# Kernel tuning notes

Measured on AMD Instinct MI355X. Metric: run time of the kernel, lower is better.

The kernel has to match this reference:

```python
import jax, jax.numpy as jnp
import numpy as np

NENV, SEQ, LATENT = 4096, 128, 64
EMB, HID = 256, 1024
SA = 2  # state_action_size


def setup_inputs() -> dict:
    key = jax.random.key(0)
    ks = jax.random.split(key, 8)
    def w(k, shape):
        return (jax.random.normal(k, shape, jnp.float32) / np.sqrt(shape[0])).astype(jnp.float32)
    return {
        "z": jax.random.normal(ks[0], (NENV, SEQ, LATENT), jnp.float32),
        "rnn_hxs": jnp.zeros((NENV, HID), jnp.float32),
        "w1": w(ks[1], (SA + LATENT, 32)), "b1": jnp.zeros((32,), jnp.float32),
        "w2": w(ks[2], (32, EMB)),          "b2": jnp.zeros((EMB,), jnp.float32),
        "wih": w(ks[3], (EMB, 3 * HID)),    "bih": jnp.zeros((3 * HID,), jnp.float32),
        "whh": w(ks[4], (HID, 3 * HID)),    "bhh": jnp.zeros((3 * HID,), jnp.float32),
        "w3": w(ks[5], (HID, HID // 2)),    "b3": jnp.zeros((HID // 2,), jnp.float32),
        "w4": w(ks[6], (HID // 2, SA)),     "b4": jnp.zeros((SA,), jnp.float32),
    }


def _gru_cell(x, h, wih, whh, bih, bhh):
    # PyTorch nn.GRU single-step semantics.
    gi = x @ wih + bih                    # [n, 3H]
    gh = h @ whh + bhh                    # [n, 3H]
    i_r, i_z, i_n = jnp.split(gi, 3, axis=-1)
    h_r, h_z, h_n = jnp.split(gh, 3, axis=-1)
    r = jax.nn.sigmoid(i_r + h_r)
    u = jax.nn.sigmoid(i_z + h_z)
    n = jnp.tanh(i_n + r * h_n)
    return (1.0 - u) * n + u * h


def reference(z, rnn_hxs, w1, b1, w2, b2, wih, bih, whh, bhh, w3, b3, w4, b4):
    zt = jnp.transpose(z, (1, 0, 2))                     # [S, N, latent]
    state0 = -2.0 * jnp.ones((z.shape[0], SA), z.dtype)  # initial fake action/state

    def step(carry, z_t):
        state, h = carry
        x = jnp.concatenate([state, z_t], axis=-1)       # [N, 2+latent]
        x = jax.nn.relu(x @ w1 + b1)
        x = jax.nn.relu(x @ w2 + b2)                     # mlp_in -> [N, EMB]
        h = _gru_cell(x, h, wih, whh, bih, bhh)          # [N, HID]
        o = jax.nn.relu(h @ w3 + b3)
        o = jnp.tanh(o @ w4 + b4)                        # output_linear -> [N, 2]
        return (o, h), o

    (_, h_new), outs = jax.lax.scan(step, (state0, rnn_hxs), zt)
    # original returns outputs.permute(1,0,2) -> [nenv, seq, 2], plus new hidden
    return jnp.transpose(outs, (1, 0, 2)), h_new
```

## Files before the change

kernel.cpp:

```cpp
#include <hip/hip_runtime.h>
#include <cstdint>
#include <cstddef>

#define NENV 4096
#define SEQ  128
#define LATENT 64
#define EMB  256
#define HID  1024
#define SA   2

typedef _Float16 half8 __attribute__((ext_vector_type(8)));
typedef float f32x4 __attribute__((ext_vector_type(4)));

__device__ __forceinline__ float sigmoid_f(float x){ return 1.0f/(1.0f + __expf(-x)); }

__device__ __forceinline__ void dma16(const void* g, void* l){
  __builtin_amdgcn_global_load_lds(
      (const __attribute__((address_space(1))) void*)g,
      (__attribute__((address_space(3))) void*)l, 16, 0, 0);
}

__device__ __forceinline__ f32x4 mfma16(half8 a, half8 b, f32x4 c){
  return __builtin_amdgcn_mfma_f32_16x16x32_f16(a, b, c, 0, 0, 0);
}

__global__ void transpose_cvt_kernel(const float* __restrict__ in, _Float16* __restrict__ out,
                                     int K, int C){
  int n = K*C;
  for (int i = blockIdx.x*blockDim.x + threadIdx.x; i < n; i += gridDim.x*blockDim.x){
    int c = i / K;
    int k = i - c*K;
    out[i] = (_Float16)in[(size_t)k*C + c];
  }
}

__global__ void init_h_kernel(const float* __restrict__ rnn, _Float16* __restrict__ h16){
  int n = NENV*HID;
  for (int i = blockIdx.x*blockDim.x + threadIdx.x; i < n; i += gridDim.x*blockDim.x){
    h16[i] = (_Float16)rnn[i];
  }
}

__global__ __launch_bounds__(256, 4) void gru_kernel(
    const _Float16* __restrict__ x2h, const _Float16* __restrict__ hcur,
    const _Float16* __restrict__ wihT, const _Float16* __restrict__ whhT,
    const float* __restrict__ bih, const float* __restrict__ bhh,
    _Float16* __restrict__ hnxt, float* __restrict__ hout)
{
  __shared__ half8 sA[256];
  __shared__ half8 sB[3][256];
  const int tid = threadIdx.x;
  const int lane = tid & 63, wave = tid >> 6;
  const int m = lane & 15, q = lane >> 4, n0 = wave*16;
  const int row = tid >> 2, seg = tid & 3;

  const int id = blockIdx.x;
  const int colg = (id & 7)*2 + ((id >> 3) & 1);
  const int rowg = id >> 4;
  const int r0 = rowg*64, c0 = colg*64;

  f32x4 accR[4], accZ[4], accNi[4], accNh[4];
#pragma unroll
  for (int i = 0; i < 4; ++i){
    accR[i] = (f32x4){0.f,0.f,0.f,0.f};
    accZ[i] = (f32x4){0.f,0.f,0.f,0.f};
    accNi[i] = (f32x4){0.f,0.f,0.f,0.f};
    accNh[i] = (f32x4){0.f,0.f,0.f,0.f};
  }

  char* dA  = (char*)&sA[wave*64];
  char* dB0 = (char*)&sB[0][wave*64];
  char* dB1 = (char*)&sB[1][wave*64];
  char* dB2 = (char*)&sB[2][wave*64];

#pragma unroll
  for (int phase = 0; phase < 2; ++phase){
    const _Float16* A = phase ? hcur : x2h;
    const _Float16* W = phase ? whhT : wihT;
    const int K = phase ? HID : EMB;
    f32x4* accN = phase ? accNh : accNi;

    const _Float16* gA  = A + (size_t)(r0 + row)*K + seg*8;
    const _Float16* gB0 = W + (size_t)(0*HID + c0 + row)*K + seg*8;
    const _Float16* gB1 = W + (size_t)(1*HID + c0 + row)*K + seg*8;
    const _Float16* gB2 = W + (size_t)(2*HID + c0 + row)*K + seg*8;

    for (int k0 = 0; k0 < K; k0 += 32){
      dma16(gA, dA); dma16(gB0, dB0); dma16(gB1, dB1); dma16(gB2, dB2);
      gA += 32; gB0 += 32; gB1 += 32; gB2 += 32;
      __syncthreads();
      half8 b0 = sB[0][(n0+m)*4 + q];
      half8 b1 = sB[1][(n0+m)*4 + q];
      half8 b2 = sB[2][(n0+m)*4 + q];
#pragma unroll
      for (int mt = 0; mt < 4; ++mt){
        half8 a = sA[(mt*16 + m)*4 + q];
        accR[mt] = mfma16(a, b0, accR[mt]);
        accZ[mt] = mfma16(a, b1, accZ[mt]);
        accN[mt] = mfma16(a, b2, accN[mt]);
      }
      __syncthreads();
    }
  }

  const int gc = c0 + n0 + m;
  const float b_r  = bih[gc]         + bhh[gc];
  const float b_z  = bih[gc + HID]   + bhh[gc + HID];
  const float b_in = bih[gc + 2*HID];
  const float b_hn = bhh[gc + 2*HID];
#pragma unroll
  for (int mt = 0; mt < 4; ++mt){
#pragma unroll
    for (int r = 0; r < 4; ++r){
      int grow = r0 + mt*16 + q*4 + r;
      float rr = sigmoid_f(accR[mt][r] + b_r);
      float u  = sigmoid_f(accZ[mt][r] + b_z);
      float nn = tanhf(accNi[mt][r] + b_in + rr*(accNh[mt][r] + b_hn));
      size_t idx = (size_t)grow*HID + gc;
      float hold = (float)hcur[idx];
      float hnew = (1.0f - u)*nn + u*hold;
      hnxt[idx] = (_Float16)hnew;
      if (hout) hout[idx] = hnew;
    }
  }
}

__global__ __launch_bounds__(256, 4) void out1_kernel(
    const _Float16* __restrict__ h16, const _Float16* __restrict__ w3T,
    const float* __restrict__ b3, _Float16* __restrict__ o1)
{
  __shared__ half8 sA[256];
  __shared__ half8 sB[256];
  const int tid = threadIdx.x;
  const int lane = tid & 63, wave = tid >> 6;
  const int m = lane & 15, q = lane >> 4, n0 = wave*16;
  const int row = tid >> 2, seg = tid & 3;

  const int id = blockIdx.x;
  const int colg = id & 7;
  const int rowg = id >> 3;
  const int r0 = rowg*64, c0 = colg*64;

  f32x4 acc[4];
#pragma unroll
  for (int i = 0; i < 4; ++i) acc[i] = (f32x4){0.f,0.f,0.f,0.f};

  char* dA = (char*)&sA[wave*64];
  char* dB = (char*)&sB[wave*64];
  const _Float16* gA = h16 + (size_t)(r0 + row)*HID + seg*8;
  const _Float16* gB = w3T + (size_t)(c0 + row)*HID + seg*8;

  for (int k0 = 0; k0 < HID; k0 += 32){
    dma16(gA, dA); dma16(gB, dB);
    gA += 32; gB += 32;
    __syncthreads();
    half8 b = sB[(n0+m)*4 + q];
#pragma unroll
    for (int mt = 0; mt < 4; ++mt){
      half8 a = sA[(mt*16 + m)*4 + q];
      acc[mt] = mfma16(a, b, acc[mt]);
    }
    __syncthreads();
  }

  const int gc = c0 + n0 + m;
  const float bb = b3[gc];
#pragma unroll
  for (int mt = 0; mt < 4; ++mt){
#pragma unroll
    for (int r = 0; r < 4; ++r){
      int grow = r0 + mt*16 + q*4 + r;
      o1[(size_t)grow*(HID/2) + gc] = (_Float16)fmaxf(acc[mt][r] + bb, 0.f);
    }
  }
}

__global__ void tail_head_kernel(
    const _Float16* __restrict__ o1, const float* __restrict__ w4, const float* __restrict__ b4,
    const float* __restrict__ z,  const float* __restrict__ w1, const float* __restrict__ b1,
    const float* __restrict__ w2, const float* __restrict__ b2,
    _Float16* __restrict__ x2h, float* __restrict__ out, int t, int mode)
{
  __shared__ float sw2[32*256];
  __shared__ float sw1[66*32];
  __shared__ float sz[16][64];
  __shared__ float sx1[16][32];
  __shared__ float sst[16][2];
  const int tid = threadIdx.x;
  const int r0 = blockIdx.x*16;

  if (mode != 2){
    for (int i = tid; i < 66*32; i += 256) sw1[i] = w1[i];
    for (int i = tid; i < 32*256; i += 256) sw2[i] = w2[i];
    int zt = (mode == 0) ? 0 : (t + 1);
    for (int i = tid; i < 16*64; i += 256){
      int r = i >> 6, k = i & 63;
      sz[r][k] = z[(size_t)(r0 + r)*SEQ*LATENT + zt*LATENT + k];
    }
  }

  if (mode != 0){
    int r = tid >> 4, p = tid & 15;
    const _Float16* orow = o1 + (size_t)(r0 + r)*(HID/2);
    float a0 = 0.f, a1 = 0.f;
    for (int k = p*32; k < p*32 + 32; ++k){
      float v = (float)orow[k];
      a0 += v*w4[k*2];
      a1 += v*w4[k*2 + 1];
    }
#pragma unroll
    for (int off = 1; off < 16; off <<= 1){
      a0 += __shfl_xor(a0, off);
      a1 += __shfl_xor(a1, off);
    }
    if (p == 0){
      a0 = tanhf(a0 + b4[0]);
      a1 = tanhf(a1 + b4[1]);
      out[(size_t)(r0 + r)*SEQ*SA + t*SA + 0] = a0;
      out[(size_t)(r0 + r)*SEQ*SA + t*SA + 1] = a1;
      sst[r][0] = a0; sst[r][1] = a1;
    }
  } else {
    if (tid < 32) sst[tid >> 1][tid & 1] = -2.0f;
  }
  __syncthreads();

  if (mode != 2){
    for (int it = tid; it < 16*32; it += 256){
      int r = it >> 5, j = it & 31;
      float acc = b1[j];
      acc += sst[r][0]*sw1[0*32 + j] + sst[r][1]*sw1[1*32 + j];
#pragma unroll 8
      for (int k = 0; k < 64; ++k) acc += sz[r][k]*sw1[(k + 2)*32 + j];
      sx1[r][j] = fmaxf(acc, 0.f);
    }
    __syncthreads();
    int col = tid;
    for (int r = 0; r < 16; ++r){
      float acc = b2[col];
#pragma unroll
      for (int k = 0; k < 32; ++k) acc += sx1[r][k]*sw2[k*256 + col];
      x2h[(size_t)(r0 + r)*EMB + col] = (_Float16)fmaxf(acc, 0.f);
    }
  }
}

extern "C" void kernel_launch(void* const* d_in, const int* in_sizes, int n_in,
                              void* d_out, int out_size, void* d_ws, size_t ws_size,
                              hipStream_t stream) {
  const float* z   = (const float*)d_in[0];
  const float* rnn = (const float*)d_in[1];
  const float* w1  = (const float*)d_in[2];
  const float* b1  = (const float*)d_in[3];
  const float* w2  = (const float*)d_in[4];
  const float* b2  = (const float*)d_in[5];
  const float* wih = (const float*)d_in[6];
  const float* bih = (const float*)d_in[7];
  const float* whh = (const float*)d_in[8];
  const float* bhh = (const float*)d_in[9];
  const float* w3  = (const float*)d_in[10];
  const float* b3  = (const float*)d_in[11];
  const float* w4  = (const float*)d_in[12];
  const float* b4  = (const float*)d_in[13];
  float* out = (float*)d_out;

  char* ws = (char*)d_ws;
  _Float16* wihT = (_Float16*)ws;                 ws += (size_t)3*HID*EMB*2;
  _Float16* whhT = (_Float16*)ws;                 ws += (size_t)3*HID*HID*2;
  _Float16* w3T  = (_Float16*)ws;                 ws += (size_t)(HID/2)*HID*2;
  _Float16* h16a = (_Float16*)ws;                 ws += (size_t)NENV*HID*2;
  _Float16* h16b = (_Float16*)ws;                 ws += (size_t)NENV*HID*2;
  _Float16* x2h  = (_Float16*)ws;                 ws += (size_t)NENV*EMB*2;
  _Float16* o1   = (_Float16*)ws;                 ws += (size_t)NENV*(HID/2)*2;

  transpose_cvt_kernel<<<512, 256, 0, stream>>>(wih, wihT, EMB, 3*HID);
  transpose_cvt_kernel<<<1024, 256, 0, stream>>>(whh, whhT, HID, 3*HID);
  transpose_cvt_kernel<<<256, 256, 0, stream>>>(w3, w3T, HID, HID/2);
  init_h_kernel<<<1024, 256, 0, stream>>>(rnn, h16a);

  tail_head_kernel<<<NENV/16, 256, 0, stream>>>(o1, w4, b4, z, w1, b1, w2, b2, x2h, out, 0, 0);

  float* hfinal = out + (size_t)NENV*SEQ*SA;
  for (int t = 0; t < SEQ; ++t){
    _Float16* hc = (t & 1) ? h16b : h16a;
    _Float16* hn = (t & 1) ? h16a : h16b;
    gru_kernel<<<1024, 256, 0, stream>>>(x2h, hc, wihT, whhT, bih, bhh, hn,
                                         (t == SEQ - 1) ? hfinal : nullptr);
    out1_kernel<<<512, 256, 0, stream>>>(hn, w3T, b3, o1);
    tail_head_kernel<<<NENV/16, 256, 0, stream>>>(o1, w4, b4, z, w1, b1, w2, b2, x2h, out,
                                                  t, (t < SEQ - 1) ? 1 : 2);
  }
}
```

Baseline: 10.90 ms.

## Enlarge GRU and output GEMM tiles to 128 rows and 64-deep K steps

The GRU and first output-layer GEMM kernels now compute 128x64 output tiles instead of 64x64 and stage 64 elements of K per barrier pair instead of 32. Each weight fragment is reused across twice as many rows and there are half as many barriers per K sweep, cutting weight traffic and sync overhead. The cost is twice the accumulator registers (launch bounds lowered to 2 blocks), more LDS per block, and half as many blocks (512 and 256), which may leave some of the 256 CUs idle or lower occupancy.

```diff
diff --git a/kernel.cpp b/kernel.cpp
--- a/kernel.cpp
+++ b/kernel.cpp
@@ -41,67 +41,86 @@
   }
 }
 
-__global__ __launch_bounds__(256, 4) void gru_kernel(
+__device__ __forceinline__ void gru_phase(
+    const _Float16* __restrict__ A, const _Float16* __restrict__ W, int K,
+    int r0, int c0, int tid, int wave, int m, int q, int n0,
+    half8* sA, half8* sB, f32x4* accR, f32x4* accZ, f32x4* accN)
+{
+  const int row64 = tid >> 2, seg = tid & 3;
+  const _Float16* gA0 = A + (size_t)(r0 +  0 + row64)*K +  0 + seg*8;
+  const _Float16* gA1 = A + (size_t)(r0 + 64 + row64)*K +  0 + seg*8;
+  const _Float16* gA2 = A + (size_t)(r0 +  0 + row64)*K + 32 + seg*8;
+  const _Float16* gA3 = A + (size_t)(r0 + 64 + row64)*K + 32 + seg*8;
+  const _Float16* gB0 = W + (size_t)(0*HID + c0 + row64)*K +  0 + seg*8;
+  const _Float16* gB1 = W + (size_t)(0*HID + c0 + row64)*K + 32 + seg*8;
+  const _Float16* gB2 = W + (size_t)(1*HID + c0 + row64)*K +  0 + seg*8;
+  const _Float16* gB3 = W + (size_t)(1*HID + c0 + row64)*K + 32 + seg*8;
+  const _Float16* gB4 = W + (size_t)(2*HID + c0 + row64)*K +  0 + seg*8;
+  const _Float16* gB5 = W + (size_t)(2*HID + c0 + row64)*K + 32 + seg*8;
+
+  char* dA0 = (char*)&sA[0*256 + wave*64];
+  char* dA1 = (char*)&sA[1*256 + wave*64];
+  char* dA2 = (char*)&sA[2*256 + wave*64];
+  char* dA3 = (char*)&sA[3*256 + wave*64];
+  char* dB0 = (char*)&sB[0*256 + wave*64];
+  char* dB1 = (char*)&sB[1*256 + wave*64];
+  char* dB2 = (char*)&sB[2*256 + wave*64];
+  char* dB3 = (char*)&sB[3*256 + wave*64];
+  char* dB4 = (char*)&sB[4*256 + wave*64];
+  char* dB5 = (char*)&sB[5*256 + wave*64];
+
+  for (int k0 = 0; k0 < K; k0 += 64){
+    dma16(gA0, dA0); dma16(gA1, dA1); dma16(gA2, dA2); dma16(gA3, dA3);
+    dma16(gB0, dB0); dma16(gB1, dB1); dma16(gB2, dB2);
+    dma16(gB3, dB3); dma16(gB4, dB4); dma16(gB5, dB5);
+    gA0 += 64; gA1 += 64; gA2 += 64; gA3 += 64;
+    gB0 += 64; gB1 += 64; gB2 += 64; gB3 += 64; gB4 += 64; gB5 += 64;
+    __syncthreads();
+#pragma unroll
+    for (int c = 0; c < 2; ++c){
+      half8 b0 = sB[0*512 + c*256 + (n0+m)*4 + q];
+      half8 b1 = sB[1*512 + c*256 + (n0+m)*4 + q];
+      half8 b2 = sB[2*512 + c*256 + (n0+m)*4 + q];
+#pragma unroll
+      for (int mt = 0; mt < 8; ++mt){
+        half8 a = sA[c*512 + (mt*16 + m)*4 + q];
+        accR[mt] = mfma16(a, b0, accR[mt]);
+        accZ[mt] = mfma16(a, b1, accZ[mt]);
+        accN[mt] = mfma16(a, b2, accN[mt]);
+      }
+    }
+    __syncthreads();
+  }
+}
+
+__global__ __launch_bounds__(256, 2) void gru_kernel(
     const _Float16* __restrict__ x2h, const _Float16* __restrict__ hcur,
     const _Float16* __restrict__ wihT, const _Float16* __restrict__ whhT,
     const float* __restrict__ bih, const float* __restrict__ bhh,
     _Float16* __restrict__ hnxt, float* __restrict__ hout)
 {
-  __shared__ half8 sA[256];
-  __shared__ half8 sB[3][256];
+  __shared__ half8 sA[1024];
+  __shared__ half8 sB[1536];
   const int tid = threadIdx.x;
   const int lane = tid & 63, wave = tid >> 6;
   const int m = lane & 15, q = lane >> 4, n0 = wave*16;
-  const int row = tid >> 2, seg = tid & 3;
 
   const int id = blockIdx.x;
   const int colg = (id & 7)*2 + ((id >> 3) & 1);
   const int rowg = id >> 4;
-  const int r0 = rowg*64, c0 = colg*64;
-
-  f32x4 accR[4], accZ[4], accNi[4], accNh[4];
-#pragma unroll
-  for (int i = 0; i < 4; ++i){
+  const int r0 = rowg*128, c0 = colg*64;
+
+  f32x4 accR[8], accZ[8], accNi[8], accNh[8];
+#pragma unroll
+  for (int i = 0; i < 8; ++i){
     accR[i] = (f32x4){0.f,0.f,0.f,0.f};
     accZ[i] = (f32x4){0.f,0.f,0.f,0.f};
     accNi[i] = (f32x4){0.f,0.f,0.f,0.f};
     accNh[i] = (f32x4){0.f,0.f,0.f,0.f};
   }
 
-  char* dA  = (char*)&sA[wave*64];
-  char* dB0 = (char*)&sB[0][wave*64];
-  char* dB1 = (char*)&sB[1][wave*64];
-  char* dB2 = (char*)&sB[2][wave*64];
-
-#pragma unroll
-  for (int phase = 0; phase < 2; ++phase){
-    const _Float16* A = phase ? hcur : x2h;
-    const _Float16* W = phase ? whhT : wihT;
-    const int K = phase ? HID : EMB;
-    f32x4* accN = phase ? accNh : accNi;
-
-    const _Float16* gA  = A + (size_t)(r0 + row)*K + seg*8;
-    const _Float16* gB0 = W + (size_t)(0*HID + c0 + row)*K + seg*8;
-    const _Float16* gB1 = W + (size_t)(1*HID + c0 + row)*K + seg*8;
-    const _Float16* gB2 = W + (size_t)(2*HID + c0 + row)*K + seg*8;
-
-    for (int k0 = 0; k0 < K; k0 += 32){
-      dma16(gA, dA); dma16(gB0, dB0); dma16(gB1, dB1); dma16(gB2, dB2);
-      gA += 32; gB0 += 32; gB1 += 32; gB2 += 32;
-      __syncthreads();
-      half8 b0 = sB[0][(n0+m)*4 + q];
-      half8 b1 = sB[1][(n0+m)*4 + q];
-      half8 b2 = sB[2][(n0+m)*4 + q];
-#pragma unroll
-      for (int mt = 0; mt < 4; ++mt){
-        half8 a = sA[(mt*16 + m)*4 + q];
-        accR[mt] = mfma16(a, b0, accR[mt]);
-        accZ[mt] = mfma16(a, b1, accZ[mt]);
-        accN[mt] = mfma16(a, b2, accN[mt]);
-      }
-      __syncthreads();
-    }
-  }
+  gru_phase(x2h,  wihT, EMB, r0, c0, tid, wave, m, q, n0, sA, sB, accR, accZ, accNi);
+  gru_phase(hcur, whhT, HID, r0, c0, tid, wave, m, q, n0, sA, sB, accR, accZ, accNh);
 
   const int gc = c0 + n0 + m;
   const float b_r  = bih[gc]         + bhh[gc];
@@ -109,7 +128,7 @@
   const float b_in = bih[gc + 2*HID];
   const float b_hn = bhh[gc + 2*HID];
 #pragma unroll
-  for (int mt = 0; mt < 4; ++mt){
+  for (int mt = 0; mt < 8; ++mt){
 #pragma unroll
     for (int r = 0; r < 4; ++r){
       int grow = r0 + mt*16 + q*4 + r;
@@ -125,40 +144,53 @@
   }
 }
 
-__global__ __launch_bounds__(256, 4) void out1_kernel(
+__global__ __launch_bounds__(256, 2) void out1_kernel(
     const _Float16* __restrict__ h16, const _Float16* __restrict__ w3T,
     const float* __restrict__ b3, _Float16* __restrict__ o1)
 {
-  __shared__ half8 sA[256];
-  __shared__ half8 sB[256];
+  __shared__ half8 sA[1024];
+  __shared__ half8 sB[512];
   const int tid = threadIdx.x;
   const int lane = tid & 63, wave = tid >> 6;
   const int m = lane & 15, q = lane >> 4, n0 = wave*16;
-  const int row = tid >> 2, seg = tid & 3;
+  const int row64 = tid >> 2, seg = tid & 3;
 
   const int id = blockIdx.x;
   const int colg = id & 7;
   const int rowg = id >> 3;
-  const int r0 = rowg*64, c0 = colg*64;
-
-  f32x4 acc[4];
-#pragma unroll
-  for (int i = 0; i < 4; ++i) acc[i] = (f32x4){0.f,0.f,0.f,0.f};
-
-  char* dA = (char*)&sA[wave*64];
-  char* dB = (char*)&sB[wave*64];
-  const _Float16* gA = h16 + (size_t)(r0 + row)*HID + seg*8;
-  const _Float16* gB = w3T + (size_t)(c0 + row)*HID + seg*8;
-
-  for (int k0 = 0; k0 < HID; k0 += 32){
-    dma16(gA, dA); dma16(gB, dB);
-    gA += 32; gB += 32;
-    __syncthreads();
-    half8 b = sB[(n0+m)*4 + q];
-#pragma unroll
-    for (int mt = 0; mt < 4; ++mt){
-      half8 a = sA[(mt*16 + m)*4 + q];
-      acc[mt] = mfma16(a, b, acc[mt]);
+  const int r0 = rowg*128, c0 = colg*64;
+
+  f32x4 acc[8];
+#pragma unroll
+  for (int i = 0; i < 8; ++i) acc[i] = (f32x4){0.f,0.f,0.f,0.f};
+
+  const _Float16* gA0 = h16 + (size_t)(r0 +  0 + row64)*HID +  0 + seg*8;
+  const _Float16* gA1 = h16 + (size_t)(r0 + 64 + row64)*HID +  0 + seg*8;
+  const _Float16* gA2 = h16 + (size_t)(r0 +  0 + row64)*HID + 32 + seg*8;
+  const _Float16* gA3 = h16 + (size_t)(r0 + 64 + row64)*HID + 32 + seg*8;
+  const _Float16* gB0 = w3T + (size_t)(c0 + row64)*HID +  0 + seg*8;
+  const _Float16* gB1 = w3T + (size_t)(c0 + row64)*HID + 32 + seg*8;
+
+  char* dA0 = (char*)&sA[0*256 + wave*64];
+  char* dA1 = (char*)&sA[1*256 + wave*64];
+  char* dA2 = (char*)&sA[2*256 + wave*64];
+  char* dA3 = (char*)&sA[3*256 + wave*64];
+  char* dB0 = (char*)&sB[0*256 + wave*64];
+  char* dB1 = (char*)&sB[1*256 + wave*64];
+
+  for (int k0 = 0; k0 < HID; k0 += 64){
+    dma16(gA0, dA0); dma16(gA1, dA1); dma16(gA2, dA2); dma16(gA3, dA3);
+    dma16(gB0, dB0); dma16(gB1, dB1);
+    gA0 += 64; gA1 += 64; gA2 += 64; gA3 += 64; gB0 += 64; gB1 += 64;
+    __syncthreads();
+#pragma unroll
+    for (int c = 0; c < 2; ++c){
+      half8 b = sB[c*256 + (n0+m)*4 + q];
+#pragma unroll
+      for (int mt = 0; mt < 8; ++mt){
+        half8 a = sA[c*512 + (mt*16 + m)*4 + q];
+        acc[mt] = mfma16(a, b, acc[mt]);
+      }
     }
     __syncthreads();
   }
@@ -166,7 +198,7 @@
   const int gc = c0 + n0 + m;
   const float bb = b3[gc];
 #pragma unroll
-  for (int mt = 0; mt < 4; ++mt){
+  for (int mt = 0; mt < 8; ++mt){
 #pragma unroll
     for (int r = 0; r < 4; ++r){
       int grow = r0 + mt*16 + q*4 + r;
@@ -284,9 +316,9 @@
   for (int t = 0; t < SEQ; ++t){
     _Float16* hc = (t & 1) ? h16b : h16a;
     _Float16* hn = (t & 1) ? h16a : h16b;
-    gru_kernel<<<1024, 256, 0, stream>>>(x2h, hc, wihT, whhT, bih, bhh, hn,
-                                         (t == SEQ - 1) ? hfinal : nullptr);
-    out1_kernel<<<512, 256, 0, stream>>>(hn, w3T, b3, o1);
+    gru_kernel<<<512, 256, 0, stream>>>(x2h, hc, wihT, whhT, bih, bhh, hn,
+                                        (t == SEQ - 1) ? hfinal : nullptr);
+    out1_kernel<<<256, 256, 0, stream>>>(hn, w3T, b3, o1);
     tail_head_kernel<<<NENV/16, 256, 0, stream>>>(o1, w4, b4, z, w1, b1, w2, b2, x2h, out,
                                                   t, (t < SEQ - 1) ? 1 : 2);
   }
```

After: 10.91 ms. About the same (+0.1%).

## Triple-buffer GEMM loads with swizzled LDS and larger GRU row tiles

Applied to the files above, without the earlier changes.

Both the GRU and output GEMM kernels now use a three-stage LDS ring with async global-to-LDS DMA issued two iterations ahead. They wait on vmcnt with a single barrier per k-step, where before each step had two full syncthreads and no prefetch. An XOR-like slot swizzle is applied to the LDS layout to avoid bank conflicts on the half8 fragment reads. The GRU kernel tile doubles to 128 rows, halving the grid and reusing each weight tile across more rows, at the cost of more accumulator registers and lower occupancy (launch bounds drop to 2).

```diff
diff --git a/kernel.cpp b/kernel.cpp
--- a/kernel.cpp
+++ b/kernel.cpp
@@ -12,6 +12,9 @@
 typedef _Float16 half8 __attribute__((ext_vector_type(8)));
 typedef float f32x4 __attribute__((ext_vector_type(4)));
 
+#define WAITVM(n) asm volatile("s_waitcnt vmcnt(" #n ")" ::: "memory")
+#define BARRIER() { __builtin_amdgcn_s_barrier(); asm volatile("" ::: "memory"); }
+
 __device__ __forceinline__ float sigmoid_f(float x){ return 1.0f/(1.0f + __expf(-x)); }
 
 __device__ __forceinline__ void dma16(const void* g, void* l){
@@ -23,6 +26,9 @@
 __device__ __forceinline__ f32x4 mfma16(half8 a, half8 b, f32x4 c){
   return __builtin_amdgcn_mfma_f32_16x16x32_f16(a, b, c, 0, 0, 0);
 }
+
+__device__ __forceinline__ int seg_for_slot(int R, int p){ return (p - R - (R >> 2)) & 3; }
+__device__ __forceinline__ int phys_slot(int R, int q){ return R*4 + ((q + R + (R >> 2)) & 3); }
 
 __global__ void transpose_cvt_kernel(const float* __restrict__ in, _Float16* __restrict__ out,
                                      int K, int C){
@@ -41,67 +47,86 @@
   }
 }
 
-__global__ __launch_bounds__(256, 4) void gru_kernel(
+template<int K, int NIT>
+__device__ __forceinline__ void gru_phase(
+    const _Float16* __restrict__ A, const _Float16* __restrict__ W,
+    int r0, int c0, int tid, int wave,
+    const int* pa, int pb, half8* sBuf,
+    f32x4* accR, f32x4* accZ, f32x4* accN)
+{
+  const int RA0 = tid >> 2,        PA0 = tid & 3;
+  const int RA1 = 64 + (tid >> 2), PA1 = tid & 3;
+  const int RB  = tid >> 2,        PB  = tid & 3;
+  const _Float16* gA0 = A + (size_t)(r0 + RA0)*K + seg_for_slot(RA0, PA0)*8;
+  const _Float16* gA1 = A + (size_t)(r0 + RA1)*K + seg_for_slot(RA1, PA1)*8;
+  const int sgb = seg_for_slot(RB, PB);
+  const _Float16* gB0 = W + (size_t)(0*HID + c0 + RB)*K + sgb*8;
+  const _Float16* gB1 = W + (size_t)(1*HID + c0 + RB)*K + sgb*8;
+  const _Float16* gB2 = W + (size_t)(2*HID + c0 + RB)*K + sgb*8;
+
+  auto issue = [&](int bi){
+    char* base = (char*)sBuf + (size_t)bi*1280*16;
+    dma16(gA0, base + (size_t)(0    + wave*64)*16);
+    dma16(gA1, base + (size_t)(256  + wave*64)*16);
+    dma16(gB0, base + (size_t)(512  + wave*64)*16);
+    dma16(gB1, base + (size_t)(768  + wave*64)*16);
+    dma16(gB2, base + (size_t)(1024 + wave*64)*16);
+    gA0 += 32; gA1 += 32; gB0 += 32; gB1 += 32; gB2 += 32;
+  };
+
+  issue(0); issue(1);
+#pragma unroll
+  for (int it = 0; it < NIT; ++it){
+    if (it < NIT - 1) { WAITVM(5); } else { WAITVM(0); }
+    BARRIER();
+    if (it + 2 < NIT) issue((it + 2) % 3);
+    const half8* buf = sBuf + (it % 3)*1280;
+    half8 b0 = buf[512  + pb];
+    half8 b1 = buf[768  + pb];
+    half8 b2 = buf[1024 + pb];
+#pragma unroll
+    for (int mt = 0; mt < 8; ++mt){
+      half8 a = buf[pa[mt]];
+      accR[mt] = mfma16(a, b0, accR[mt]);
+      accZ[mt] = mfma16(a, b1, accZ[mt]);
+      accN[mt] = mfma16(a, b2, accN[mt]);
+    }
+  }
+  __syncthreads();
+}
+
+__global__ __launch_bounds__(256, 2) void gru_kernel(
     const _Float16* __restrict__ x2h, const _Float16* __restrict__ hcur,
     const _Float16* __restrict__ wihT, const _Float16* __restrict__ whhT,
     const float* __restrict__ bih, const float* __restrict__ bhh,
     _Float16* __restrict__ hnxt, float* __restrict__ hout)
 {
-  __shared__ half8 sA[256];
-  __shared__ half8 sB[3][256];
+  __shared__ half8 sBuf[3*1280];
   const int tid = threadIdx.x;
   const int lane = tid & 63, wave = tid >> 6;
   const int m = lane & 15, q = lane >> 4, n0 = wave*16;
-  const int row = tid >> 2, seg = tid & 3;
 
   const int id = blockIdx.x;
   const int colg = (id & 7)*2 + ((id >> 3) & 1);
   const int rowg = id >> 4;
-  const int r0 = rowg*64, c0 = colg*64;
-
-  f32x4 accR[4], accZ[4], accNi[4], accNh[4];
-#pragma unroll
-  for (int i = 0; i < 4; ++i){
+  const int r0 = rowg*128, c0 = colg*64;
+
+  int pa[8];
+#pragma unroll
+  for (int mt = 0; mt < 8; ++mt) pa[mt] = phys_slot(mt*16 + m, q);
+  const int pb = phys_slot(n0 + m, q);
+
+  f32x4 accR[8], accZ[8], accNi[8], accNh[8];
+#pragma unroll
+  for (int i = 0; i < 8; ++i){
     accR[i] = (f32x4){0.f,0.f,0.f,0.f};
     accZ[i] = (f32x4){0.f,0.f,0.f,0.f};
     accNi[i] = (f32x4){0.f,0.f,0.f,0.f};
     accNh[i] = (f32x4){0.f,0.f,0.f,0.f};
   }
 
-  char* dA  = (char*)&sA[wave*64];
-  char* dB0 = (char*)&sB[0][wave*64];
-  char* dB1 = (char*)&sB[1][wave*64];
-  char* dB2 = (char*)&sB[2][wave*64];
-
-#pragma unroll
-  for (int phase = 0; phase < 2; ++phase){
-    const _Float16* A = phase ? hcur : x2h;
-    const _Float16* W = phase ? whhT : wihT;
-    const int K = phase ? HID : EMB;
-    f32x4* accN = phase ? accNh : accNi;
-
-    const _Float16* gA  = A + (size_t)(r0 + row)*K + seg*8;
-    const _Float16* gB0 = W + (size_t)(0*HID + c0 + row)*K + seg*8;
-    const _Float16* gB1 = W + (size_t)(1*HID + c0 + row)*K + seg*8;
-    const _Float16* gB2 = W + (size_t)(2*HID + c0 + row)*K + seg*8;
-
-    for (int k0 = 0; k0 < K; k0 += 32){
-      dma16(gA, dA); dma16(gB0, dB0); dma16(gB1, dB1); dma16(gB2, dB2);
-      gA += 32; gB0 += 32; gB1 += 32; gB2 += 32;
-      __syncthreads();
-      half8 b0 = sB[0][(n0+m)*4 + q];
-      half8 b1 = sB[1][(n0+m)*4 + q];
-      half8 b2 = sB[2][(n0+m)*4 + q];
-#pragma unroll
-      for (int mt = 0; mt < 4; ++mt){
-        half8 a = sA[(mt*16 + m)*4 + q];
-        accR[mt] = mfma16(a, b0, accR[mt]);
-        accZ[mt] = mfma16(a, b1, accZ[mt]);
-        accN[mt] = mfma16(a, b2, accN[mt]);
-      }
-      __syncthreads();
-    }
-  }
+  gru_phase<EMB, EMB/32>(x2h,  wihT, r0, c0, tid, wave, pa, pb, sBuf, accR, accZ, accNi);
+  gru_phase<HID, HID/32>(hcur, whhT, r0, c0, tid, wave, pa, pb, sBuf, accR, accZ, accNh);
 
   const int gc = c0 + n0 + m;
   const float b_r  = bih[gc]         + bhh[gc];
@@ -109,7 +134,7 @@
   const float b_in = bih[gc + 2*HID];
   const float b_hn = bhh[gc + 2*HID];
 #pragma unroll
-  for (int mt = 0; mt < 4; ++mt){
+  for (int mt = 0; mt < 8; ++mt){
 #pragma unroll
     for (int r = 0; r < 4; ++r){
       int grow = r0 + mt*16 + q*4 + r;
@@ -129,38 +154,50 @@
     const _Float16* __restrict__ h16, const _Float16* __restrict__ w3T,
     const float* __restrict__ b3, _Float16* __restrict__ o1)
 {
-  __shared__ half8 sA[256];
-  __shared__ half8 sB[256];
+  __shared__ half8 sBuf[3*512];
   const int tid = threadIdx.x;
   const int lane = tid & 63, wave = tid >> 6;
   const int m = lane & 15, q = lane >> 4, n0 = wave*16;
-  const int row = tid >> 2, seg = tid & 3;
 
   const int id = blockIdx.x;
   const int colg = id & 7;
   const int rowg = id >> 3;
   const int r0 = rowg*64, c0 = colg*64;
 
+  int pa[4];
+#pragma unroll
+  for (int mt = 0; mt < 4; ++mt) pa[mt] = phys_slot(mt*16 + m, q);
+  const int pb = phys_slot(n0 + m, q);
+
   f32x4 acc[4];
 #pragma unroll
   for (int i = 0; i < 4; ++i) acc[i] = (f32x4){0.f,0.f,0.f,0.f};
 
-  char* dA = (char*)&sA[wave*64];
-  char* dB = (char*)&sB[wave*64];
-  const _Float16* gA = h16 + (size_t)(r0 + row)*HID + seg*8;
-  const _Float16* gB = w3T + (size_t)(c0 + row)*HID + seg*8;
-
-  for (int k0 = 0; k0 < HID; k0 += 32){
-    dma16(gA, dA); dma16(gB, dB);
+  const int R = tid >> 2, P = tid & 3;
+  const int sg = seg_for_slot(R, P);
+  const _Float16* gA = h16 + (size_t)(r0 + R)*HID + sg*8;
+  const _Float16* gB = w3T + (size_t)(c0 + R)*HID + sg*8;
+
+  auto issue = [&](int bi){
+    char* base = (char*)sBuf + (size_t)bi*512*16;
+    dma16(gA, base + (size_t)(0   + wave*64)*16);
+    dma16(gB, base + (size_t)(256 + wave*64)*16);
     gA += 32; gB += 32;
-    __syncthreads();
-    half8 b = sB[(n0+m)*4 + q];
+  };
+
+  issue(0); issue(1);
+#pragma unroll
+  for (int it = 0; it < 32; ++it){
+    if (it < 31) { WAITVM(2); } else { WAITVM(0); }
+    BARRIER();
+    if (it + 2 < 32) issue((it + 2) % 3);
+    const half8* buf = sBuf + (it % 3)*512;
+    half8 b = buf[256 + pb];
 #pragma unroll
     for (int mt = 0; mt < 4; ++mt){
-      half8 a = sA[(mt*16 + m)*4 + q];
+      half8 a = buf[pa[mt]];
       acc[mt] = mfma16(a, b, acc[mt]);
     }
-    __syncthreads();
   }
 
   const int gc = c0 + n0 + m;
@@ -284,8 +321,8 @@
   for (int t = 0; t < SEQ; ++t){
     _Float16* hc = (t & 1) ? h16b : h16a;
     _Float16* hn = (t & 1) ? h16a : h16b;
-    gru_kernel<<<1024, 256, 0, stream>>>(x2h, hc, wihT, whhT, bih, bhh, hn,
-                                         (t == SEQ - 1) ? hfinal : nullptr);
+    gru_kernel<<<512, 256, 0, stream>>>(x2h, hc, wihT, whhT, bih, bhh, hn,
+                                        (t == SEQ - 1) ? hfinal : nullptr);
     out1_kernel<<<512, 256, 0, stream>>>(hn, w3T, b3, o1);
     tail_head_kernel<<<NENV/16, 256, 0, stream>>>(o1, w4, b4, z, w1, b1, w2, b2, x2h, out,
                                                   t, (t < SEQ - 1) ? 1 : 2);
```

Result: faster. 9.895 ms (-9.2%).
